# Optimization experiments

Measured on AMD Instinct MI355X. Metric: run time of the kernel, lower is better.

The kernel has to match this reference:

```python
import jax, jax.numpy as jnp
import numpy as np

N_NODES = 100000
N_EDGES = 3200000
N_IN = 512
N_H = 256

def setup_inputs() -> dict:
    key = jax.random.key(0)
    ks = jax.random.split(key, 8)
    features = jax.random.normal(ks[0], (N_NODES, N_IN), dtype=jnp.float32)
    src = jax.random.randint(ks[1], (N_EDGES,), 0, N_NODES, dtype=jnp.int32)
    dst = jax.random.randint(ks[2], (N_EDGES,), 0, N_NODES, dtype=jnp.int32)
    W1 = jax.random.normal(ks[3], (N_IN, N_H), dtype=jnp.float32) / np.sqrt(N_IN)
    b1 = jnp.zeros((N_H,), dtype=jnp.float32)
    a1 = jnp.full((N_H,), 0.25, dtype=jnp.float32)  # PReLU init
    W2 = jax.random.normal(ks[4], (N_H, N_H), dtype=jnp.float32) / np.sqrt(N_H)
    b2 = jnp.zeros((N_H,), dtype=jnp.float32)
    a2 = jnp.full((N_H,), 0.25, dtype=jnp.float32)
    return {"features": features, "src": src, "dst": dst,
            "W1": W1, "b1": b1, "a1": a1, "W2": W2, "b2": b2, "a2": a2}

def _degree_norms(src, dst, n_nodes):
    ones = jnp.ones(src.shape[0], dtype=jnp.float32)
    out_deg = jax.ops.segment_sum(ones, src, num_segments=n_nodes)
    in_deg = jax.ops.segment_sum(ones, dst, num_segments=n_nodes)
    # DGL clamps degree to min 1 for norm='both'
    norm_src = jax.lax.rsqrt(jnp.maximum(out_deg, 1.0))  # [N]
    norm_dst = jax.lax.rsqrt(jnp.maximum(in_deg, 1.0))   # [N]
    return norm_src, norm_dst

def _graph_conv(x, src, dst, norm_src, norm_dst, W, b, a):
    # DGL GraphConv norm='both': h = Dd^-1/2 * A^T (Ds^-1/2 * x W) + b, then PReLU
    h = (x * norm_src[:, None]) @ W                     # [N, out]
    agg = jax.ops.segment_sum(h[src], dst, num_segments=x.shape[0])  # SpMM gather/scatter
    h = agg * norm_dst[:, None] + b
    return jnp.maximum(h, 0.0) + a * jnp.minimum(h, 0.0)  # PReLU per-channel

def reference(features, src, dst, W1, b1, a1, W2, b2, a2):
    norm_src, norm_dst = _degree_norms(src, dst, features.shape[0])
    h = _graph_conv(features, src, dst, norm_src, norm_dst, W1, b1, a1)
    h = _graph_conv(h, src, dst, norm_src, norm_dst, W2, b2, a2)
    return h
```

## Files before the change

### kernel.cpp

```cpp
#include <hip/hip_runtime.h>
#include <hip/hip_bf16.h>

typedef unsigned short u16;
typedef short s16x8 __attribute__((ext_vector_type(8)));
typedef u16 u16x4 __attribute__((ext_vector_type(4)));
typedef u16 u16x8 __attribute__((ext_vector_type(8)));
typedef float f32x4 __attribute__((ext_vector_type(4)));

#define BSHIFT 10

__device__ __forceinline__ u16 f2bf(float f) {
    __hip_bfloat16 b = __float2bfloat16(f);
    return __builtin_bit_cast(u16, b);
}
__device__ __forceinline__ float bf2f(u16 u) {
    unsigned int x = ((unsigned int)u) << 16;
    return __builtin_bit_cast(float, x);
}


__global__ __launch_bounds__(256) void bhist_k(const int* __restrict__ src,
                                               const int* __restrict__ dst,
                                               int* __restrict__ bcntA,
                                               int* __restrict__ bcntB,
                                               int E, int chunk) {
    __shared__ int hA[128], hB[128];
    const int base = blockIdx.x * chunk;
    const int end = (base + chunk) < E ? (base + chunk) : E;
    if (threadIdx.x < 128) { hA[threadIdx.x] = 0; hB[threadIdx.x] = 0; }
    __syncthreads();
    for (int i = base + threadIdx.x; i < end; i += 256) {
        atomicAdd(&hA[dst[i] >> BSHIFT], 1);
        atomicAdd(&hB[src[i] >> BSHIFT], 1);
    }
    __syncthreads();
    if (threadIdx.x < 128) {
        if (hA[threadIdx.x]) atomicAdd(&bcntA[threadIdx.x], hA[threadIdx.x]);
        if (hB[threadIdx.x]) atomicAdd(&bcntB[threadIdx.x], hB[threadIdx.x]);
    }
}

__global__ void bscan_k(const int* __restrict__ bcntA, const int* __restrict__ bcntB,
                        int* __restrict__ bbaseA, int* __restrict__ bbaseB,
                        int* __restrict__ bcurA, int* __restrict__ bcurB,
                        int* __restrict__ row_ptr, int NB, int N, int E) {
    __shared__ int tA[128], tB[128];
    const int t = threadIdx.x;
    int vA = (t < NB) ? bcntA[t] : 0;
    int vB = (t < NB) ? bcntB[t] : 0;
    tA[t] = vA; tB[t] = vB;
    __syncthreads();
    for (int d = 1; d < 128; d <<= 1) {
        int aA = (t >= d) ? tA[t - d] : 0;
        int aB = (t >= d) ? tB[t - d] : 0;
        __syncthreads();
        tA[t] += aA; tB[t] += aB;
        __syncthreads();
    }
    if (t < NB) {
        int eA = tA[t] - vA, eB = tB[t] - vB;
        bbaseA[t] = eA; bcurA[t] = eA;
        bbaseB[t] = eB; bcurB[t] = eB;
    } else if (t == NB) {
        bbaseA[NB] = E; bbaseB[NB] = E;
    }
    if (t == 0) row_ptr[N] = E;
}

__global__ __launch_bounds__(256) void part_k(const int* __restrict__ src,
                                              const int* __restrict__ dst,
                                              int* __restrict__ bcurA,
                                              int* __restrict__ bcurB,
                                              int2* __restrict__ pairs,
                                              int* __restrict__ sb,
                                              int E, int chunk) {
    __shared__ int hA[128], hB[128];
    const int base = blockIdx.x * chunk;
    const int end = (base + chunk) < E ? (base + chunk) : E;
    if (threadIdx.x < 128) { hA[threadIdx.x] = 0; hB[threadIdx.x] = 0; }
    __syncthreads();
    for (int i = base + threadIdx.x; i < end; i += 256) {
        atomicAdd(&hA[dst[i] >> BSHIFT], 1);
        atomicAdd(&hB[src[i] >> BSHIFT], 1);
    }
    __syncthreads();
    if (threadIdx.x < 128) {
        int c = hA[threadIdx.x];
        hA[threadIdx.x] = c ? atomicAdd(&bcurA[threadIdx.x], c) : 0;
        c = hB[threadIdx.x];
        hB[threadIdx.x] = c ? atomicAdd(&bcurB[threadIdx.x], c) : 0;
    }
    __syncthreads();
    for (int i = base + threadIdx.x; i < end; i += 256) {
        int d = dst[i], s = src[i];
        int posA = atomicAdd(&hA[d >> BSHIFT], 1);
        int2 pr; pr.x = s; pr.y = d;
        pairs[posA] = pr;
        int posB = atomicAdd(&hB[s >> BSHIFT], 1);
        sb[posB] = s;
    }
}

__global__ __launch_bounds__(256) void bcsr_k(const int2* __restrict__ pairs,
                                              const int* __restrict__ bbase,
                                              int* __restrict__ row_ptr,
                                              int* __restrict__ din,
                                              int* __restrict__ col, int N) {
    __shared__ int hist[1024];
    __shared__ int cur[1024];
    __shared__ int psum[256];
    const int b = blockIdx.x;
    const int beg = bbase[b], end = bbase[b + 1];
    const int nbase = b << BSHIFT;
    const int nlen = (N - nbase) < 1024 ? (N - nbase) : 1024;
    const int t = threadIdx.x;
#pragma unroll
    for (int j = 0; j < 4; j++) hist[t * 4 + j] = 0;
    __syncthreads();
    for (int i = beg + t; i < end; i += 256)
        atomicAdd(&hist[pairs[i].y - nbase], 1);
    __syncthreads();
    int h0 = hist[4 * t], h1 = hist[4 * t + 1], h2 = hist[4 * t + 2], h3 = hist[4 * t + 3];
    int s = h0 + h1 + h2 + h3;
    psum[t] = s;
    __syncthreads();
    for (int d = 1; d < 256; d <<= 1) {
        int add = (t >= d) ? psum[t - d] : 0;
        __syncthreads();
        psum[t] += add;
        __syncthreads();
    }
    int e0 = psum[t] - s;
    int e1 = e0 + h0, e2 = e1 + h1, e3 = e2 + h2;
    cur[4 * t] = beg + e0; cur[4 * t + 1] = beg + e1;
    cur[4 * t + 2] = beg + e2; cur[4 * t + 3] = beg + e3;
    if (4 * t + 0 < nlen) { row_ptr[nbase + 4 * t + 0] = beg + e0; din[nbase + 4 * t + 0] = h0; }
    if (4 * t + 1 < nlen) { row_ptr[nbase + 4 * t + 1] = beg + e1; din[nbase + 4 * t + 1] = h1; }
    if (4 * t + 2 < nlen) { row_ptr[nbase + 4 * t + 2] = beg + e2; din[nbase + 4 * t + 2] = h2; }
    if (4 * t + 3 < nlen) { row_ptr[nbase + 4 * t + 3] = beg + e3; din[nbase + 4 * t + 3] = h3; }
    __syncthreads();
    for (int i = beg + t; i < end; i += 256) {
        int2 p = pairs[i];
        int pos = atomicAdd(&cur[p.y - nbase], 1);
        col[pos] = p.x;
    }
}

__global__ __launch_bounds__(256) void bdeg_k(const int* __restrict__ sb,
                                              const int* __restrict__ bbase,
                                              int* __restrict__ dout, int N) {
    __shared__ int hist[1024];
    const int b = blockIdx.x;
    const int beg = bbase[b], end = bbase[b + 1];
    const int nbase = b << BSHIFT;
    const int nlen = (N - nbase) < 1024 ? (N - nbase) : 1024;
    for (int i = threadIdx.x; i < 1024; i += 256) hist[i] = 0;
    __syncthreads();
    for (int i = beg + threadIdx.x; i < end; i += 256)
        atomicAdd(&hist[sb[i] - nbase], 1);
    __syncthreads();
    for (int i = threadIdx.x; i < nlen; i += 256) dout[nbase + i] = hist[i];
}

__global__ void norms_k(const int* __restrict__ dout, const int* __restrict__ din,
                        float* __restrict__ ns, float* __restrict__ nd, int n) {
    int i = blockIdx.x * blockDim.x + threadIdx.x;
    if (i < n) {
        ns[i] = 1.0f / sqrtf(fmaxf((float)dout[i], 1.0f));
        nd[i] = 1.0f / sqrtf(fmaxf((float)din[i], 1.0f));
    }
}

__global__ void convt_k(const float* __restrict__ W, u16* __restrict__ Wt, int K, int Nn) {
    int i = blockIdx.x * blockDim.x + threadIdx.x;
    if (i < K * Nn) {
        int n = i / K, k = i - n * K;
        Wt[i] = f2bf(W[(size_t)k * Nn + n]);
    }
}


template <int K, bool AF32>
__global__ __launch_bounds__(512) void gemm_k(const void* __restrict__ Ap,
                                              const float* __restrict__ nsrc,
                                              const u16* __restrict__ Bt,
                                              u16* __restrict__ C, int M) {
    constexpr int BKt = 64;
    __shared__ u16 Al[128 * BKt];
    __shared__ u16 Bl[256 * BKt];
    const int tid = threadIdx.x, lane = tid & 63, wid = tid >> 6;
    const int wr = wid >> 2, wc = wid & 3;
    const int l15 = lane & 15, lhi = lane >> 4;
    const int bm = blockIdx.x * 128;
    f32x4 acc[4][4] = {};

    for (int k0 = 0; k0 < K; k0 += BKt) {
#pragma unroll
        for (int i = 0; i < 2; i++) {
            int G = i * 512 + tid, row = G >> 3, gk = G & 7;
            int grow = bm + row;
            grow = grow < M ? grow : M - 1;
            u16x8 w;
            if constexpr (AF32) {
                const float* A = (const float*)Ap;
                const f32x4 v0 = *(const f32x4*)(A + (size_t)grow * K + k0 + gk * 8);
                const f32x4 v1 = *(const f32x4*)(A + (size_t)grow * K + k0 + gk * 8 + 4);
                const float ns = nsrc[grow];
                w[0] = f2bf(v0[0] * ns); w[1] = f2bf(v0[1] * ns);
                w[2] = f2bf(v0[2] * ns); w[3] = f2bf(v0[3] * ns);
                w[4] = f2bf(v1[0] * ns); w[5] = f2bf(v1[1] * ns);
                w[6] = f2bf(v1[2] * ns); w[7] = f2bf(v1[3] * ns);
            } else {
                const u16* A = (const u16*)Ap;
                w = *(const u16x8*)(A + (size_t)grow * K + k0 + gk * 8);
            }
            int idx = (row * BKt + gk * 8) ^ ((row & 7) << 3);
            *(u16x8*)(Al + idx) = w;
        }
#pragma unroll
        for (int i = 0; i < 4; i++) {
            int G = i * 512 + tid, row = G >> 3, gk = G & 7;
            u16x8 wb = *(const u16x8*)(Bt + (size_t)row * K + k0 + gk * 8);
            int idx = (row * BKt + gk * 8) ^ ((row & 7) << 3);
            *(u16x8*)(Bl + idx) = wb;
        }
        __syncthreads();

        s16x8 af[2][4], bfr[2][4];
#pragma unroll
        for (int kk = 0; kk < 2; kk++) {
#pragma unroll
            for (int mi = 0; mi < 4; mi++) {
                int row = wr * 64 + mi * 16 + l15;
                int idx = (row * BKt + kk * 32 + lhi * 8) ^ ((row & 7) << 3);
                af[kk][mi] = *(const s16x8*)(Al + idx);
            }
#pragma unroll
            for (int ni = 0; ni < 4; ni++) {
                int n = wc * 64 + ni * 16 + l15;
                int idx = (n * BKt + kk * 32 + lhi * 8) ^ ((n & 7) << 3);
                bfr[kk][ni] = *(const s16x8*)(Bl + idx);
            }
        }
#pragma unroll
        for (int kk = 0; kk < 2; kk++)
#pragma unroll
            for (int mi = 0; mi < 4; mi++)
#pragma unroll
                for (int ni = 0; ni < 4; ni++)
                    acc[mi][ni] = __builtin_amdgcn_mfma_f32_16x16x32_bf16(
                        af[kk][mi], bfr[kk][ni], acc[mi][ni], 0, 0, 0);
        __syncthreads();
    }

#pragma unroll
    for (int mi = 0; mi < 4; mi++) {
#pragma unroll
        for (int r = 0; r < 4; r++) {
            int grow = bm + wr * 64 + mi * 16 + lhi * 4 + r;
            if (grow < M) {
#pragma unroll
                for (int ni = 0; ni < 4; ni++) {
                    int gcol = wc * 64 + ni * 16 + l15;
                    C[(size_t)grow * 256 + gcol] = f2bf(acc[mi][ni][r]);
                }
            }
        }
    }
}


__global__ __launch_bounds__(256) void agg_k(const u16* __restrict__ h,
                                             const int* __restrict__ rp,
                                             const int* __restrict__ col,
                                             const float* __restrict__ nd,
                                             const float* __restrict__ bias,
                                             const float* __restrict__ alpha,
                                             const float* __restrict__ ns,
                                             u16* __restrict__ obf, float* __restrict__ of,
                                             int n) {
    int w = (blockIdx.x * blockDim.x + threadIdx.x) >> 5;
    if (w >= n) return;
    const int c0 = (threadIdx.x & 31) * 8;
    const int beg = rp[w], end = rp[w + 1];

    float a0[8] = {}, a1[8] = {}, a2[8] = {}, a3[8] = {};

    int p = beg;
    for (; p + 7 < end; p += 8) {
        int s0 = col[p], s1 = col[p + 1], s2 = col[p + 2], s3 = col[p + 3];
        int s4 = col[p + 4], s5 = col[p + 5], s6 = col[p + 6], s7 = col[p + 7];
        u16x8 v0 = *(const u16x8*)(h + (size_t)s0 * 256 + c0);
        u16x8 v1 = *(const u16x8*)(h + (size_t)s1 * 256 + c0);
        u16x8 v2 = *(const u16x8*)(h + (size_t)s2 * 256 + c0);
        u16x8 v3 = *(const u16x8*)(h + (size_t)s3 * 256 + c0);
        u16x8 v4 = *(const u16x8*)(h + (size_t)s4 * 256 + c0);
        u16x8 v5 = *(const u16x8*)(h + (size_t)s5 * 256 + c0);
        u16x8 v6 = *(const u16x8*)(h + (size_t)s6 * 256 + c0);
        u16x8 v7 = *(const u16x8*)(h + (size_t)s7 * 256 + c0);
#pragma unroll
        for (int j = 0; j < 8; j++) {
            a0[j] += bf2f(v0[j]);
            a1[j] += bf2f(v1[j]);
            a2[j] += bf2f(v2[j]);
            a3[j] += bf2f(v3[j]);
        }
#pragma unroll
        for (int j = 0; j < 8; j++) {
            a0[j] += bf2f(v4[j]);
            a1[j] += bf2f(v5[j]);
            a2[j] += bf2f(v6[j]);
            a3[j] += bf2f(v7[j]);
        }
    }
    for (; p + 3 < end; p += 4) {
        int s0 = col[p], s1 = col[p + 1], s2 = col[p + 2], s3 = col[p + 3];
        u16x8 v0 = *(const u16x8*)(h + (size_t)s0 * 256 + c0);
        u16x8 v1 = *(const u16x8*)(h + (size_t)s1 * 256 + c0);
        u16x8 v2 = *(const u16x8*)(h + (size_t)s2 * 256 + c0);
        u16x8 v3 = *(const u16x8*)(h + (size_t)s3 * 256 + c0);
#pragma unroll
        for (int j = 0; j < 8; j++) {
            a0[j] += bf2f(v0[j]);
            a1[j] += bf2f(v1[j]);
            a2[j] += bf2f(v2[j]);
            a3[j] += bf2f(v3[j]);
        }
    }
    for (; p < end; p++) {
        int s = col[p];
        u16x8 v = *(const u16x8*)(h + (size_t)s * 256 + c0);
#pragma unroll
        for (int j = 0; j < 8; j++) a0[j] += bf2f(v[j]);
    }
#pragma unroll
    for (int j = 0; j < 8; j++) a0[j] = (a0[j] + a1[j]) + (a2[j] + a3[j]);

    const float ndv = nd[w];
    const f32x4 bv0 = *(const f32x4*)(bias + c0);
    const f32x4 bv1 = *(const f32x4*)(bias + c0 + 4);
    const f32x4 al0 = *(const f32x4*)(alpha + c0);
    const f32x4 al1 = *(const f32x4*)(alpha + c0 + 4);
    float bb[8] = {bv0[0], bv0[1], bv0[2], bv0[3], bv1[0], bv1[1], bv1[2], bv1[3]};
    float aa[8] = {al0[0], al0[1], al0[2], al0[3], al1[0], al1[1], al1[2], al1[3]};
#pragma unroll
    for (int j = 0; j < 8; j++) {
        float s = a0[j] * ndv + bb[j];
        a0[j] = s > 0.f ? s : aa[j] * s;
    }

    if (obf) {
        const float nsv = ns[w];
        u16x8 o;
#pragma unroll
        for (int j = 0; j < 8; j++) o[j] = f2bf(a0[j] * nsv);
        *(u16x8*)(obf + (size_t)w * 256 + c0) = o;
    } else {
        f32x4 o0, o1;
        o0[0] = a0[0]; o0[1] = a0[1]; o0[2] = a0[2]; o0[3] = a0[3];
        o1[0] = a0[4]; o1[1] = a0[5]; o1[2] = a0[6]; o1[3] = a0[7];
        *(f32x4*)(of + (size_t)w * 256 + c0) = o0;
        *(f32x4*)(of + (size_t)w * 256 + c0 + 4) = o1;
    }
}


extern "C" void kernel_launch(void* const* d_in, const int* in_sizes, int n_in,
                              void* d_out, int out_size, void* d_ws, size_t ws_size,
                              hipStream_t stream) {
    const float* feat = (const float*)d_in[0];
    const int* src = (const int*)d_in[1];
    const int* dst = (const int*)d_in[2];
    const float* W1 = (const float*)d_in[3];
    const float* b1 = (const float*)d_in[4];
    const float* a1 = (const float*)d_in[5];
    const float* W2 = (const float*)d_in[6];
    const float* b2 = (const float*)d_in[7];
    const float* a2 = (const float*)d_in[8];
    float* out = (float*)d_out;

    const int N = in_sizes[0] / 512;
    const int E = in_sizes[1];
    const int NB = (N + (1 << BSHIFT) - 1) >> BSHIFT;

    char* ws = (char*)d_ws;
    size_t off = 0;
    auto take = [&](size_t bytes) {
        size_t o = off;
        off += (bytes + 255) & ~(size_t)255;
        return o;
    };
    int* deg_out = (int*)(ws + take((size_t)N * 4));
    int* deg_in = (int*)(ws + take((size_t)N * 4));
    float* nsrc = (float*)(ws + take((size_t)N * 4));
    float* ndst = (float*)(ws + take((size_t)N * 4));
    int* row_ptr = (int*)(ws + take((size_t)(N + 1) * 4));
    int* bcnt = (int*)(ws + take(1024));
    int* bcntA = bcnt, * bcntB = bcnt + 128;
    int* bbaseA = (int*)(ws + take(512));
    int* bbaseB = (int*)(ws + take(512));
    int* bcurA = (int*)(ws + take(512));
    int* bcurB = (int*)(ws + take(512));
    int* col = (int*)(ws + take((size_t)E * 4));
    u16* W1t = (u16*)(ws + take((size_t)512 * 256 * 2));
    u16* W2t = (u16*)(ws + take((size_t)256 * 256 * 2));
    u16* h = (u16*)(ws + take((size_t)N * 256 * 2));
    u16* x2 = (u16*)(ws + take((size_t)N * 256 * 2));
    int2* pairs = (int2*)h;
    int* sb = (int*)x2;

    hipMemsetAsync(bcnt, 0, 1024, stream);

    const int chunk = 4096;
    bhist_k<<<(E + chunk - 1) / chunk, 256, 0, stream>>>(src, dst, bcntA, bcntB, E, chunk);
    bscan_k<<<1, 128, 0, stream>>>(bcntA, bcntB, bbaseA, bbaseB, bcurA, bcurB, row_ptr, NB, N, E);
    part_k<<<(E + chunk - 1) / chunk, 256, 0, stream>>>(src, dst, bcurA, bcurB, pairs, sb, E, chunk);
    bcsr_k<<<NB, 256, 0, stream>>>(pairs, bbaseA, row_ptr, deg_in, col, N);
    bdeg_k<<<NB, 256, 0, stream>>>(sb, bbaseB, deg_out, N);
    norms_k<<<(N + 255) / 256, 256, 0, stream>>>(deg_out, deg_in, nsrc, ndst, N);

    convt_k<<<(512 * 256 + 255) / 256, 256, 0, stream>>>(W1, W1t, 512, 256);
    convt_k<<<(256 * 256 + 255) / 256, 256, 0, stream>>>(W2, W2t, 256, 256);

    dim3 gg((N + 127) / 128);
    int aggBlocks = (N * 32 + 255) / 256;

    gemm_k<512, true><<<gg, 512, 0, stream>>>(feat, nsrc, W1t, h, N);
    agg_k<<<aggBlocks, 256, 0, stream>>>(h, row_ptr, col, ndst, b1, a1, nsrc, x2, nullptr, N);
    gemm_k<256, false><<<gg, 512, 0, stream>>>(x2, nullptr, W2t, h, N);
    agg_k<<<aggBlocks, 256, 0, stream>>>(h, row_ptr, col, ndst, b2, a2, nullptr, nullptr, out, N);
}
```

Before: 761.5 us.

## Sort CSR neighbor lists per row and software-pipeline gather index loads

Adds a per-row bitonic sort kernel (one wavefront per row, with an insertion-sort fallback for rows above 128 entries) so each destination's source indices are in ascending order. The intent is better L2/TLB locality when the aggregation kernels gather rows of h. The aggregation loop now loads the next batch of eight column indices before accumulating the current batch, and adds a launch-bounds occupancy hint. The sort is an extra pass over 3.2M edges and its cost has to be outweighed by more cache-friendly gathers in the two aggregation kernels.

```diff
diff --git a/kernel.cpp b/kernel.cpp
--- a/kernel.cpp
+++ b/kernel.cpp
@@ -160,6 +160,49 @@
         atomicAdd(&hist[sb[i] - nbase], 1);
     __syncthreads();
     for (int i = threadIdx.x; i < nlen; i += 256) dout[nbase + i] = hist[i];
+}
+
+__global__ __launch_bounds__(256) void sortrow_k(const int* __restrict__ rp,
+                                                 int* __restrict__ col, int n) {
+    int w = (blockIdx.x * blockDim.x + threadIdx.x) >> 6;
+    if (w >= n) return;
+    const int lane = threadIdx.x & 63;
+    const int beg = rp[w], end = rp[w + 1];
+    const int deg = end - beg;
+    if (deg <= 1) return;
+    if (deg <= 128) {
+        const int INF = 0x7fffffff;
+        int a = (lane < deg) ? col[beg + lane] : INF;
+        int b = (64 + lane < deg) ? col[beg + 64 + lane] : INF;
+#pragma unroll
+        for (int k = 2; k <= 128; k <<= 1) {
+#pragma unroll
+            for (int j = k >> 1; j > 0; j >>= 1) {
+                if (j >= 64) {
+                    int lo = a < b ? a : b, hi = a < b ? b : a;
+                    a = lo; b = hi;
+                } else {
+                    int pa = __shfl_xor(a, j);
+                    int pb = __shfl_xor(b, j);
+                    bool lower = ((lane & j) == 0);
+                    bool asc_a = ((lane & k) == 0);
+                    bool asc_b = (((lane + 64) & k) == 0);
+                    int mna = a < pa ? a : pa, mxa = a < pa ? pa : a;
+                    int mnb = b < pb ? b : pb, mxb = b < pb ? pb : b;
+                    a = (lower == asc_a) ? mna : mxa;
+                    b = (lower == asc_b) ? mnb : mxb;
+                }
+            }
+        }
+        if (lane < deg) col[beg + lane] = a;
+        if (64 + lane < deg) col[beg + 64 + lane] = b;
+    } else if (lane == 0) {
+        for (int i = beg + 1; i < end; i++) {
+            int v = col[i], j = i - 1;
+            while (j >= beg && col[j] > v) { col[j + 1] = col[j]; j--; }
+            col[j + 1] = v;
+        }
+    }
 }
 
 __global__ void norms_k(const int* __restrict__ dout, const int* __restrict__ din,
@@ -270,34 +313,65 @@
 }
 
 
-__global__ __launch_bounds__(256) void agg_k(const u16* __restrict__ h,
-                                             const int* __restrict__ rp,
-                                             const int* __restrict__ col,
-                                             const float* __restrict__ nd,
-                                             const float* __restrict__ bias,
-                                             const float* __restrict__ alpha,
-                                             const float* __restrict__ ns,
-                                             u16* __restrict__ obf, float* __restrict__ of,
-                                             int n) {
+__global__ __launch_bounds__(256, 4) void agg_k(const u16* __restrict__ h,
+                                                const int* __restrict__ rp,
+                                                const int* __restrict__ col,
+                                                const float* __restrict__ nd,
+                                                const float* __restrict__ bias,
+                                                const float* __restrict__ alpha,
+                                                const float* __restrict__ ns,
+                                                u16* __restrict__ obf, float* __restrict__ of,
+                                                int n) {
     int w = (blockIdx.x * blockDim.x + threadIdx.x) >> 5;
     if (w >= n) return;
     const int c0 = (threadIdx.x & 31) * 8;
     const int beg = rp[w], end = rp[w + 1];
+    const u16* __restrict__ hb = h + c0;
 
     float a0[8] = {}, a1[8] = {}, a2[8] = {}, a3[8] = {};
 
     int p = beg;
-    for (; p + 7 < end; p += 8) {
+    if (p + 7 < end) {
         int s0 = col[p], s1 = col[p + 1], s2 = col[p + 2], s3 = col[p + 3];
         int s4 = col[p + 4], s5 = col[p + 5], s6 = col[p + 6], s7 = col[p + 7];
-        u16x8 v0 = *(const u16x8*)(h + (size_t)s0 * 256 + c0);
-        u16x8 v1 = *(const u16x8*)(h + (size_t)s1 * 256 + c0);
-        u16x8 v2 = *(const u16x8*)(h + (size_t)s2 * 256 + c0);
-        u16x8 v3 = *(const u16x8*)(h + (size_t)s3 * 256 + c0);
-        u16x8 v4 = *(const u16x8*)(h + (size_t)s4 * 256 + c0);
-        u16x8 v5 = *(const u16x8*)(h + (size_t)s5 * 256 + c0);
-        u16x8 v6 = *(const u16x8*)(h + (size_t)s6 * 256 + c0);
-        u16x8 v7 = *(const u16x8*)(h + (size_t)s7 * 256 + c0);
+        while (true) {
+            u16x8 v0 = *(const u16x8*)(hb + (size_t)s0 * 256);
+            u16x8 v1 = *(const u16x8*)(hb + (size_t)s1 * 256);
+            u16x8 v2 = *(const u16x8*)(hb + (size_t)s2 * 256);
+            u16x8 v3 = *(const u16x8*)(hb + (size_t)s3 * 256);
+            u16x8 v4 = *(const u16x8*)(hb + (size_t)s4 * 256);
+            u16x8 v5 = *(const u16x8*)(hb + (size_t)s5 * 256);
+            u16x8 v6 = *(const u16x8*)(hb + (size_t)s6 * 256);
+            u16x8 v7 = *(const u16x8*)(hb + (size_t)s7 * 256);
+            p += 8;
+            bool more = (p + 7 < end);
+            if (more) {
+                s0 = col[p]; s1 = col[p + 1]; s2 = col[p + 2]; s3 = col[p + 3];
+                s4 = col[p + 4]; s5 = col[p + 5]; s6 = col[p + 6]; s7 = col[p + 7];
+            }
+#pragma unroll
+            for (int j = 0; j < 8; j++) {
+                a0[j] += bf2f(v0[j]);
+                a1[j] += bf2f(v1[j]);
+                a2[j] += bf2f(v2[j]);
+                a3[j] += bf2f(v3[j]);
+            }
+#pragma unroll
+            for (int j = 0; j < 8; j++) {
+                a0[j] += bf2f(v4[j]);
+                a1[j] += bf2f(v5[j]);
+                a2[j] += bf2f(v6[j]);
+                a3[j] += bf2f(v7[j]);
+            }
+            if (!more) break;
+        }
+    }
+    for (; p + 3 < end; p += 4) {
+        int s0 = col[p], s1 = col[p + 1], s2 = col[p + 2], s3 = col[p + 3];
+        u16x8 v0 = *(const u16x8*)(hb + (size_t)s0 * 256);
+        u16x8 v1 = *(const u16x8*)(hb + (size_t)s1 * 256);
+        u16x8 v2 = *(const u16x8*)(hb + (size_t)s2 * 256);
+        u16x8 v3 = *(const u16x8*)(hb + (size_t)s3 * 256);
 #pragma unroll
         for (int j = 0; j < 8; j++) {
             a0[j] += bf2f(v0[j]);
@@ -305,31 +379,10 @@
             a2[j] += bf2f(v2[j]);
             a3[j] += bf2f(v3[j]);
         }
-#pragma unroll
-        for (int j = 0; j < 8; j++) {
-            a0[j] += bf2f(v4[j]);
-            a1[j] += bf2f(v5[j]);
-            a2[j] += bf2f(v6[j]);
-            a3[j] += bf2f(v7[j]);
-        }
-    }
-    for (; p + 3 < end; p += 4) {
-        int s0 = col[p], s1 = col[p + 1], s2 = col[p + 2], s3 = col[p + 3];
-        u16x8 v0 = *(const u16x8*)(h + (size_t)s0 * 256 + c0);
-        u16x8 v1 = *(const u16x8*)(h + (size_t)s1 * 256 + c0);
-        u16x8 v2 = *(const u16x8*)(h + (size_t)s2 * 256 + c0);
-        u16x8 v3 = *(const u16x8*)(h + (size_t)s3 * 256 + c0);
-#pragma unroll
-        for (int j = 0; j < 8; j++) {
-            a0[j] += bf2f(v0[j]);
-            a1[j] += bf2f(v1[j]);
-            a2[j] += bf2f(v2[j]);
-            a3[j] += bf2f(v3[j]);
-        }
     }
     for (; p < end; p++) {
         int s = col[p];
-        u16x8 v = *(const u16x8*)(h + (size_t)s * 256 + c0);
+        u16x8 v = *(const u16x8*)(hb + (size_t)s * 256);
 #pragma unroll
         for (int j = 0; j < 8; j++) a0[j] += bf2f(v[j]);
     }
@@ -417,6 +470,7 @@
     part_k<<<(E + chunk - 1) / chunk, 256, 0, stream>>>(src, dst, bcurA, bcurB, pairs, sb, E, chunk);
     bcsr_k<<<NB, 256, 0, stream>>>(pairs, bbaseA, row_ptr, deg_in, col, N);
     bdeg_k<<<NB, 256, 0, stream>>>(sb, bbaseB, deg_out, N);
+    sortrow_k<<<(N * 64 + 255) / 256, 256, 0, stream>>>(row_ptr, col, N);
     norms_k<<<(N + 255) / 256, 256, 0, stream>>>(deg_out, deg_in, nsrc, ndst, N);
 
     convt_k<<<(512 * 256 + 255) / 256, 256, 0, stream>>>(W1, W1t, 512, 256);
```

Measured after the change: 825.6 us. +8.4%, slower.
